# Kernel tuning notes

Hardware: AMD Instinct MI355X
Metric: run time of the kernel (lower is better)

The kernel has to match this reference:

```python
import jax, jax.numpy as jnp
import numpy as np

N_NODES = 50000
N_EDGES = 200000
NODE_DIM = 160     # node feat dim (divisible by 5 per wrapper slicing)
EDGE_DIM = 64      # latent edge feat dim
RAW_EDGE_DIM = 8   # raw geometric edge attributes
HID = 256          # hidden dim of edge/node update MLPs
ENC_HID = 128      # hidden dim of EASP edge encoder
N_ITER = 3
ENC_IN = 2 * NODE_DIM + RAW_EDGE_DIM                 # 328
EDGE_IN = 2 * 2 * NODE_DIM + 2 * EDGE_DIM            # 768 (reattach -> factor 2)
MSG_IN = 2 * NODE_DIM + EDGE_DIM                     # 384 (reattach node + edge)


def _ln(x, g, b):
    mu = jnp.mean(x, axis=-1, keepdims=True)
    v = jnp.var(x, axis=-1, keepdims=True)
    return (x - mu) * jax.lax.rsqrt(v + 1e-5) * g + b


def setup_inputs() -> dict:
    key = jax.random.key(0)
    ks = jax.random.split(key, 24)

    def w(k, shape):
        return (jax.random.normal(k, shape, jnp.float32) / np.sqrt(shape[0])).astype(jnp.float32)

    return {
        'x': jax.random.normal(ks[0], (N_NODES, NODE_DIM), jnp.float32),
        'edge_attr': jax.random.normal(ks[1], (N_EDGES, RAW_EDGE_DIM), jnp.float32),
        # EASP edge encoder MLP
        'enc_W1': w(ks[2], (ENC_IN, ENC_HID)), 'enc_b1': jnp.zeros((ENC_HID,), jnp.float32),
        'enc_W2': w(ks[3], (ENC_HID, EDGE_DIM)), 'enc_b2': jnp.zeros((EDGE_DIM,), jnp.float32),
        # EdgeCNN edge update MLP
        'eW1': w(ks[4], (EDGE_IN, HID)), 'eb1': jnp.zeros((HID,), jnp.float32),
        'eW2': w(ks[5], (HID, EDGE_DIM)), 'eb2': jnp.zeros((EDGE_DIM,), jnp.float32),
        # AttentionNodeUpdateNet: per-edge message MLP + attention vector + node out
        'mW1': w(ks[6], (MSG_IN, HID)), 'mb1': jnp.zeros((HID,), jnp.float32),
        'att_v': w(ks[7], (HID,)),
        'nW1': w(ks[8], (HID, NODE_DIM)), 'nb1': jnp.zeros((NODE_DIM,), jnp.float32),
        # shared LayerNorms (ModuleList([layer]*n_iter) shares one layer)
        'ln_ng': jnp.ones((NODE_DIM,), jnp.float32), 'ln_nb': jnp.zeros((NODE_DIM,), jnp.float32),
        'ln_eg': jnp.ones((EDGE_DIM,), jnp.float32), 'ln_eb': jnp.zeros((EDGE_DIM,), jnp.float32),
        'edge_row': jax.random.randint(ks[9], (N_EDGES,), 0, N_NODES, jnp.int32),
        'edge_col': jax.random.randint(ks[10], (N_EDGES,), 0, N_NODES, jnp.int32),
    }


def reference(x, edge_attr, enc_W1, enc_b1, enc_W2, enc_b2, eW1, eb1, eW2, eb2,
              mW1, mb1, att_v, nW1, nb1, ln_ng, ln_nb, ln_eg, ln_eb,
              edge_row, edge_col):
    row, col = edge_row, edge_col
    # edge encoder: gather endpoints, encode raw edge attrs
    init_edge = jnp.concatenate([x[row], x[col], edge_attr], axis=1)  # [E, 328]
    init_edge = jnp.maximum(init_edge @ enc_W1 + enc_b1, 0.0) @ enc_W2 + enc_b2  # [E, 64]

    node_lat, edge_lat = x, init_edge
    for _ in range(N_ITER):
        nl = jnp.concatenate([x, node_lat], axis=1)            # reattach initial node feats [N, 320]
        el = jnp.concatenate([init_edge, edge_lat], axis=1)    # reattach initial edge feats [E, 128]
        # edge update: gather-concat-MLP
        e_in = jnp.concatenate([nl[row], nl[col], el], axis=1)  # [E, 768]
        new_edge = jnp.maximum(e_in @ eW1 + eb1, 0.0) @ eW2 + eb2  # [E, 64]
        # node update: per-edge message + segment-softmax attention + scatter agg
        msg = jnp.maximum(jnp.concatenate([nl[col], new_edge], axis=1) @ mW1 + mb1, 0.0)  # [E, 256]
        logit = jax.nn.leaky_relu(msg @ att_v, 0.2)             # [E]
        smax = jax.ops.segment_max(logit, row, num_segments=N_NODES)
        ex = jnp.exp(logit - smax[row])
        den = jax.ops.segment_sum(ex, row, num_segments=N_NODES)
        alpha = ex / (den[row] + 1e-16)
        agg = jax.ops.segment_sum(alpha[:, None] * msg, row, num_segments=N_NODES)  # [N, 256]
        new_node = agg @ nW1 + nb1                              # [N, 160]
        # residual skip + (shared) LayerNorm
        node_lat = _ln(x + new_node, ln_ng, ln_nb)
        edge_lat = _ln(init_edge + new_edge, ln_eg, ln_eb)
    return node_lat, edge_lat
```

## Files before the change

### kernel.cpp

```cpp
#include <hip/hip_runtime.h>
#include <stdint.h>

#define N_NODES 50000
#define N_EDGES 200000
#define SCAN_B 512

typedef __bf16 bf16_t;
typedef bf16_t bf16x8 __attribute__((ext_vector_type(8)));
typedef float f32x4 __attribute__((ext_vector_type(4)));

__device__ __forceinline__ float bf2f(ushort h) {
  union { unsigned int u; float f; } c; c.u = ((unsigned int)h) << 16; return c.f;
}
__device__ __forceinline__ ushort f2bf(float f) {
  union { float f; unsigned int u; } c; c.f = f;
  unsigned int r = (c.u >> 16) & 1u;
  c.u += 0x7fffu + r;
  return (ushort)(c.u >> 16);
}
__device__ __forceinline__ float wave_sum(float v) {
#pragma unroll
  for (int m = 32; m > 0; m >>= 1) v += __shfl_xor(v, m, 64);
  return v;
}

__global__ void detect_k(const ushort* x, unsigned int* flag) {
  int i = blockIdx.x * 256 + threadIdx.x;
  unsigned int cnt = 0;
  for (int j = i; j < 1000000; j += 64 * 256) {
    ushort v = x[j];
    if (((v & 0x7F80u) == 0x7F80u) && (v & 0x7Fu)) cnt++;
  }
  if (cnt) atomicAdd(flag, cnt);
}

__global__ void cvt_in_k(const void* src, ushort* dst, int n, const unsigned int* flag) {
  int i = blockIdx.x * 256 + threadIdx.x;
  if (i >= n) return;
  if (*flag >= 2) dst[i] = f2bf(((const float*)src)[i]);
  else            dst[i] = ((const ushort*)src)[i];
}

__global__ void cvt_eattr_k(const void* src, const int* perm, ushort* dst,
                            const unsigned int* flag) {
  int i = blockIdx.x * 256 + threadIdx.x;
  if (i >= N_EDGES * 8) return;
  int e = i >> 3, j = i & 7;
  size_t o = (size_t)perm[e] * 8 + j;
  if (*flag >= 2) dst[i] = f2bf(((const float*)src)[o]);
  else            dst[i] = ((const ushort*)src)[o];
}

__global__ void transpose2_k(const void* W, ushort* Bt, int k0, int Ksrc, int Kpad,
                             int Wstride, const unsigned int* flag) {
  int k = blockIdx.x * 256 + threadIdx.x;
  int n = blockIdx.y;
  if (k >= Kpad) return;
  ushort v = 0;
  if (k < Ksrc) {
    if (*flag >= 2) v = f2bf(((const float*)W)[(size_t)(k0 + k) * Wstride + n]);
    else            v = ((const ushort*)W)[(size_t)(k0 + k) * Wstride + n];
  }
  Bt[(size_t)n * Kpad + k] = v;
}

__global__ void hist_k(const int* row, int* deg) {
  int e = blockIdx.x * 256 + threadIdx.x;
  if (e < N_EDGES) atomicAdd(&deg[row[e]], 1);
}
__global__ void scan_blk_k(const int* deg, int* off, int* bsum, int n) {
  __shared__ int s[SCAN_B];
  int i = blockIdx.x * SCAN_B + threadIdx.x;
  int v = (i < n) ? deg[i] : 0;
  s[threadIdx.x] = v;
  __syncthreads();
  for (int o = 1; o < SCAN_B; o <<= 1) {
    int t = (threadIdx.x >= o) ? s[threadIdx.x - o] : 0;
    __syncthreads();
    s[threadIdx.x] += t;
    __syncthreads();
  }
  if (i < n) off[i] = s[threadIdx.x] - v;
  if (threadIdx.x == SCAN_B - 1) bsum[blockIdx.x] = s[SCAN_B - 1];
}
__global__ void scan_top_k(int* bsum, int nb) {
  __shared__ int s[128];
  int v = (threadIdx.x < nb) ? bsum[threadIdx.x] : 0;
  s[threadIdx.x] = v;
  __syncthreads();
  for (int o = 1; o < 128; o <<= 1) {
    int t = (threadIdx.x >= o) ? s[threadIdx.x - o] : 0;
    __syncthreads();
    s[threadIdx.x] += t;
    __syncthreads();
  }
  if (threadIdx.x < nb) bsum[threadIdx.x] = s[threadIdx.x] - v;
}
__global__ void scan_add_k(int* off, const int* bsum, int n) {
  int i = blockIdx.x * 256 + threadIdx.x;
  if (i < n) off[i] += bsum[i >> 9];
  if (i == 0) off[n] = N_EDGES;
}
__global__ void fill_k(const int* row, const int* off, int* cur, int* perm) {
  int e = blockIdx.x * 256 + threadIdx.x;
  if (e >= N_EDGES) return;
  int r = row[e];
  int p = off[r] + atomicAdd(&cur[r], 1);
  perm[p] = e;
}
__global__ void gather_rc_k(const int* row, const int* col, const int* perm,
                            int* rs, int* cs) {
  int e = blockIdx.x * 256 + threadIdx.x;
  if (e >= N_EDGES) return;
  int o = perm[e];
  rs[e] = row[o];
  cs[e] = col[o];
}

struct GemmP {
  const ushort* X;
  const ushort* L;
  const ushort* E2;
  const float*  Af;
  const int* row;
  const int* col;
  const ushort* Bt;
  const ushort* bias;
  const ushort* Cr;
  const ushort* Cc;
  long cst;
  ushort* outb;  long ob_stride;
  ushort* outb2; long ob2_stride;
  ushort* outS;  long oS_stride;
  int nsplit;
  float*  outf;  long of_stride;
  long e2s;
  int M, K, Nw;
};

template <int MODE>
__device__ __forceinline__ uint4 load_a8(const GemmP& p, int e, int kg) {
  if (MODE == 0) {
    return *(const uint4*)(p.E2 + (size_t)e * p.e2s + kg);
  } else if (MODE == 5) {
    if (kg < 160) return *(const uint4*)(p.X + (size_t)e * 160 + kg);
    return *(const uint4*)(p.L + (size_t)e * 160 + (kg - 160));
  } else if (MODE == 7) {
    if (kg < 160) return *(const uint4*)(p.X + (size_t)e * 160 + kg);
    uint4 z; z.x = z.y = z.z = z.w = 0u; return z;
  } else if (MODE == 8) {
    if (kg < 8) return *(const uint4*)(p.E2 + (size_t)e * 8);
    uint4 z; z.x = z.y = z.z = z.w = 0u; return z;
  } else {
    const float* s = p.Af + (size_t)e * p.K + kg;
    f32x4 f0 = *(const f32x4*)s;
    f32x4 f1 = *(const f32x4*)(s + 4);
    union { ushort r[8]; uint4 u; } o;
    o.r[0] = f2bf(f0[0]); o.r[1] = f2bf(f0[1]); o.r[2] = f2bf(f0[2]); o.r[3] = f2bf(f0[3]);
    o.r[4] = f2bf(f1[0]); o.r[5] = f2bf(f1[1]); o.r[6] = f2bf(f1[2]); o.r[7] = f2bf(f1[3]);
    return o.u;
  }
}

template <int MODE, int CI, bool RELU, int NT, bool LNN>
__global__ __launch_bounds__(256) void gemm_k(GemmP p) {
  constexpr int BR = NT / 2;
  constexpr int NTC = NT * 16;
  constexpr int CIP = NTC + 8;
  __shared__ __align__(16) ushort smem[9216 + 1152 * NT];
  ushort* Asm = smem;
  ushort* Bsm = smem + 9216;
  const int t = threadIdx.x;
  const int w = t >> 6;
  const int l = t & 63;
  const int m0 = blockIdx.y * 128;
  const int n0 = blockIdx.x * NTC;

  const int srow = t >> 1;
  const int sph = (t & 1) << 5;
  int e = m0 + srow;
  if (e >= p.M) e = p.M - 1;

  int bn_[BR], bk_[BR];
#pragma unroll
  for (int j = 0; j < BR; j++) {
    int cid = j * 256 + t;
    bn_[j] = cid >> 3;
    bk_[j] = (cid & 7) << 3;
  }

  const int mq = l & 15;
  const int qd = l >> 4;

  uint4 ar[4];
  uint4 br[BR];
  auto load_tile = [&](int k0) {
#pragma unroll
    for (int j = 0; j < 4; j++)
      ar[j] = load_a8<MODE>(p, e, k0 + sph + j * 8);
#pragma unroll
    for (int j = 0; j < BR; j++)
      br[j] = *(const uint4*)(p.Bt + (size_t)(n0 + bn_[j]) * p.K + k0 + bk_[j]);
  };

  load_tile(0);

  f32x4 acc[2][NT] = {};
  if (CI) {
#pragma unroll
    for (int mt = 0; mt < 2; mt++) {
#pragma unroll
      for (int i = 0; i < 4; i++) {
        int r = m0 + w * 32 + mt * 16 + qd * 4 + i;
        if (r >= p.M) r = p.M - 1;
        const ushort* pc = p.Cc + (size_t)p.col[r] * p.cst + n0 + mq;
        const ushort* pr = nullptr;
        if (CI == 1) pr = p.Cr + (size_t)p.row[r] * p.cst + n0 + mq;
#pragma unroll
        for (int nt = 0; nt < NT; nt++) {
          float v = bf2f(pc[nt * 16]);
          if (CI == 1) v += bf2f(pr[nt * 16]);
          acc[mt][nt][i] = v;
        }
      }
    }
  }

  const int kiters = p.K >> 6;
  for (int kt = 0; kt < kiters; kt++) {
    __syncthreads();
#pragma unroll
    for (int j = 0; j < 4; j++)
      *(uint4*)&Asm[srow * 72 + sph + j * 8] = ar[j];
#pragma unroll
    for (int j = 0; j < BR; j++)
      *(uint4*)&Bsm[bn_[j] * 72 + bk_[j]] = br[j];
    if (kt + 1 < kiters) load_tile((kt + 1) << 6);
    __syncthreads();
#pragma unroll
    for (int ph = 0; ph < 2; ph++) {
      uint4 ra0 = *(const uint4*)&Asm[(w * 32 + mq) * 72 + ph * 32 + qd * 8];
      uint4 ra1 = *(const uint4*)&Asm[(w * 32 + 16 + mq) * 72 + ph * 32 + qd * 8];
      bf16x8 af0 = __builtin_bit_cast(bf16x8, ra0);
      bf16x8 af1 = __builtin_bit_cast(bf16x8, ra1);
#pragma unroll
      for (int nt = 0; nt < NT; nt++) {
        uint4 rb = *(const uint4*)&Bsm[(nt * 16 + mq) * 72 + ph * 32 + qd * 8];
        bf16x8 bfv = __builtin_bit_cast(bf16x8, rb);
        acc[0][nt] = __builtin_amdgcn_mfma_f32_16x16x32_bf16(af0, bfv, acc[0][nt], 0, 0, 0);
        acc[1][nt] = __builtin_amdgcn_mfma_f32_16x16x32_bf16(af1, bfv, acc[1][nt], 0, 0, 0);
      }
    }
  }

  if (MODE == 4) {
    if (LNN) {
#pragma unroll
      for (int mt = 0; mt < 2; mt++) {
#pragma unroll
        for (int i = 0; i < 4; i++) {
          int r = m0 + w * 32 + mt * 16 + qd * 4 + i;
          int rc = (r < p.M) ? r : p.M - 1;
          float vals[NT];
          float s = 0.0f;
#pragma unroll
          for (int nt = 0; nt < NT; nt++) {
            int c = n0 + nt * 16 + mq;
            float v = acc[mt][nt][i] + bf2f(p.bias[c]) +
                      bf2f(p.X[(size_t)rc * p.of_stride + c]);
            vals[nt] = v; s += v;
          }
#pragma unroll
          for (int m = 1; m <= 8; m <<= 1) s += __shfl_xor(s, m, 64);
          float mu = s * (1.0f / 160.0f);
          float ss = 0.0f;
#pragma unroll
          for (int nt = 0; nt < NT; nt++) { float d = vals[nt] - mu; ss += d * d; }
#pragma unroll
          for (int m = 1; m <= 8; m <<= 1) ss += __shfl_xor(ss, m, 64);
          float inv = rsqrtf(ss * (1.0f / 160.0f) + 1e-5f);
          if (r < p.M) {
#pragma unroll
            for (int nt = 0; nt < NT; nt++) {
              int c = n0 + nt * 16 + mq;
              float o = (vals[nt] - mu) * inv * bf2f(p.Cr[c]) + bf2f(p.Cc[c]);
              p.outb[(size_t)r * p.ob_stride + c] = f2bf(o);
            }
          }
        }
      }
    } else {
#pragma unroll
      for (int mt = 0; mt < 2; mt++) {
#pragma unroll
        for (int nt = 0; nt < NT; nt++) {
          int c = n0 + nt * 16 + mq;
          float bv = bf2f(p.bias[c]);
#pragma unroll
          for (int i = 0; i < 4; i++) {
            int r = m0 + w * 32 + mt * 16 + qd * 4 + i;
            if (r >= p.M) continue;
            float v = acc[mt][nt][i] + bv;
            if (RELU) v = fmaxf(v, 0.0f);
            p.outf[(size_t)r * p.of_stride + c] = v;
          }
        }
      }
    }
  } else {
    ushort* dst = p.outb;
    long dstr = p.ob_stride;
    int nb0 = n0;
    if (p.outS && n0 >= p.nsplit) { dst = p.outS; dstr = p.oS_stride; nb0 = n0 - p.nsplit; }
    __syncthreads();
    ushort* S = smem + w * (32 * CIP);
#pragma unroll
    for (int mt = 0; mt < 2; mt++) {
#pragma unroll
      for (int nt = 0; nt < NT; nt++) {
        float bv = bf2f(p.bias[n0 + nt * 16 + mq]);
#pragma unroll
        for (int i = 0; i < 4; i++) {
          float v = acc[mt][nt][i] + bv;
          if (RELU) v = fmaxf(v, 0.0f);
          S[(mt * 16 + qd * 4 + i) * CIP + nt * 16 + mq] = f2bf(v);
        }
      }
    }
    __syncthreads();
#pragma unroll
    for (int j = 0; j < NT; j++) {
      int flat = (j * 64 + l) * 8;
      int lr = flat / NTC, cc = flat % NTC;
      int r = m0 + w * 32 + lr;
      if (r < p.M) {
        uint4 v = *(const uint4*)&S[lr * CIP + cc];
        *(uint4*)(dst + (size_t)r * dstr + nb0 + cc) = v;
        if (p.outb2) *(uint4*)(p.outb2 + (size_t)r * p.ob2_stride + n0 + cc) = v;
      }
    }
  }
}

__global__ void copy_u4_k(const uint4* s, uint4* d, int n) {
  int i = blockIdx.x * 256 + threadIdx.x;
  if (i < n) d[i] = s[i];
}

__global__ void agg_csr_k(const ushort* msg, const ushort* att, const int* off,
                          float* agg) {
  int n = blockIdx.x * 4 + (threadIdx.x >> 6);
  int l = threadIdx.x & 63;
  if (n >= N_NODES) return;
  const int s0 = off[n], s1 = off[n + 1];
  ushort4 av = *(const ushort4*)(att + l * 4);
  const float a0 = bf2f(av.x), a1 = bf2f(av.y), a2 = bf2f(av.z), a3 = bf2f(av.w);
  float maxl = -1e30f;
  for (int j = s0; j < s1; j++) {
    ushort4 m = *(const ushort4*)(msg + (size_t)j * 256 + l * 4);
    float d = bf2f(m.x) * a0 + bf2f(m.y) * a1 + bf2f(m.z) * a2 + bf2f(m.w) * a3;
    d = wave_sum(d);
    float lg = (d > 0.0f) ? d : 0.2f * d;
    maxl = fmaxf(maxl, lg);
  }
  float den = 0.0f;
  f32x4 acc = {0.0f, 0.0f, 0.0f, 0.0f};
  for (int j = s0; j < s1; j++) {
    ushort4 m = *(const ushort4*)(msg + (size_t)j * 256 + l * 4);
    float m0 = bf2f(m.x), m1 = bf2f(m.y), m2 = bf2f(m.z), m3 = bf2f(m.w);
    float d = m0 * a0 + m1 * a1 + m2 * a2 + m3 * a3;
    d = wave_sum(d);
    float lg = (d > 0.0f) ? d : 0.2f * d;
    float ex = __expf(lg - maxl);
    den += ex;
    acc[0] += ex * m0; acc[1] += ex * m1; acc[2] += ex * m2; acc[3] += ex * m3;
  }
  float inv = 1.0f / (den + 1e-16f);
  f32x4 o = {acc[0] * inv, acc[1] * inv, acc[2] * inv, acc[3] * inv};
  *(f32x4*)(agg + (size_t)n * 256 + l * 4) = o;
}

__global__ void ln_edge_k(const ushort* g, const ushort* b, ushort* el) {
  int e = blockIdx.x * 4 + (threadIdx.x >> 6);
  int l = threadIdx.x & 63;
  if (e >= N_EDGES) return;
  float v = bf2f(el[(size_t)e * 128 + l]) + bf2f(el[(size_t)e * 128 + 64 + l]);
  float mu = wave_sum(v) * (1.0f / 64.0f);
  float d = v - mu;
  float var = wave_sum(d * d) * (1.0f / 64.0f);
  float inv = rsqrtf(var + 1e-5f);
  el[(size_t)e * 128 + 64 + l] = f2bf(d * inv * bf2f(g[l]) + bf2f(b[l]));
}

__global__ void out_node_k(const ushort* nlat, void* out, const unsigned int* flag) {
  int i = blockIdx.x * 256 + threadIdx.x;
  if (i >= N_NODES * 160) return;
  if (*flag >= 2) ((float*)out)[i] = bf2f(nlat[i]);
  else            ((ushort*)out)[i] = nlat[i];
}
__global__ void out_edge_k(const ushort* el, const int* perm, void* out,
                           const unsigned int* flag) {
  int i = blockIdx.x * 256 + threadIdx.x;
  if (i >= N_EDGES * 64) return;
  int e = i >> 6, c = i & 63;
  ushort v = el[(size_t)e * 128 + 64 + c];
  size_t o = (size_t)N_NODES * 160 + (size_t)perm[e] * 64 + c;
  if (*flag >= 2) ((float*)out)[o] = bf2f(v);
  else            ((ushort*)out)[o] = v;
}

extern "C" void kernel_launch(void* const* d_in, const int* in_sizes, int n_in,
                              void* d_out, int out_size, void* d_ws, size_t ws_size,
                              hipStream_t stream) {
  const void* x_r     = d_in[0];
  const void* eattr_r = d_in[1];
  const void* encW1   = d_in[2];
  const void* encb1_r = d_in[3];
  const void* encW2   = d_in[4];
  const void* encb2_r = d_in[5];
  const void* eW1     = d_in[6];
  const void* eb1_r   = d_in[7];
  const void* eW2     = d_in[8];
  const void* eb2_r   = d_in[9];
  const void* mW1     = d_in[10];
  const void* mb1_r   = d_in[11];
  const void* attv_r  = d_in[12];
  const void* nW1     = d_in[13];
  const void* nb1_r   = d_in[14];
  const void* lnng_r  = d_in[15];
  const void* lnnb_r  = d_in[16];
  const void* lneg_r  = d_in[17];
  const void* lneb_r  = d_in[18];
  const int* erow = (const int*)d_in[19];
  const int* ecol = (const int*)d_in[20];
  (void)in_sizes; (void)n_in;

  char* ws = (char*)d_ws;
  size_t off = 0;
  auto alloc = [&](size_t bytes) -> void* {
    void* p = ws + off;
    off = (off + bytes + 511) & ~(size_t)511;
    return p;
  };
  ushort* hm   = (ushort*)alloc((size_t)N_EDGES * 256 * 2);
  ushort* el   = (ushort*)alloc((size_t)N_EDGES * 128 * 2);
  float*  agg  = (float*)alloc((size_t)N_NODES * 256 * 4);
  ushort* xc   = (ushort*)alloc((size_t)N_NODES * 160 * 2);
  ushort* nlat = (ushort*)alloc((size_t)N_NODES * 160 * 2);
  ushort* Qc   = (ushort*)alloc((size_t)N_NODES * 256 * 2);
  int* degcur  = (int*)alloc((size_t)2 * N_NODES * 4);
  int* offcsr  = (int*)alloc((size_t)(N_NODES + 1) * 4);
  int* perm    = (int*)alloc((size_t)N_EDGES * 4);
  int* rs      = (int*)alloc((size_t)N_EDGES * 4);
  int* cs      = (int*)alloc((size_t)N_EDGES * 4);
  int* bsum    = (int*)alloc((size_t)128 * 4);
  ushort* BtPe = (ushort*)alloc((size_t)256 * 192 * 2);
  ushort* BtWenc = (ushort*)alloc((size_t)128 * 64 * 2);
  ushort* BtE2 = (ushort*)alloc((size_t)64 * 128 * 2);
  ushort* BtPQ = (ushort*)alloc((size_t)768 * 320 * 2);
  ushort* BtWe = (ushort*)alloc((size_t)256 * 128 * 2);
  ushort* Bte2 = (ushort*)alloc((size_t)64 * 256 * 2);
  ushort* BtWm = (ushort*)alloc((size_t)256 * 64 * 2);
  ushort* Btn1 = (ushort*)alloc((size_t)160 * 256 * 2);
  ushort* pool = (ushort*)alloc((size_t)4096 * 2);
  unsigned int* flag = (unsigned int*)alloc(64);
  ushort* msg = hm;
  ushort* eac  = (ushort*)agg;
  ushort* Penc = (ushort*)((char*)agg + (size_t)N_EDGES * 8 * 2);
  ushort* Prc  = (ushort*)agg;
  ushort* zb   = pool + 2048;

  ushort* encb1c = pool;        ushort* encb2c = pool + 128;
  ushort* eb1c   = pool + 192;  ushort* eb2c   = pool + 448;
  ushort* mb1c   = pool + 512;  ushort* attvc  = pool + 768;
  ushort* nb1c   = pool + 1024; ushort* lnngc  = pool + 1184;
  ushort* lnnbc  = pool + 1344; ushort* lnegc  = pool + 1504;
  ushort* lnebc  = pool + 1568;

  if (off > ws_size) {
    hipMemsetAsync(d_out, 0, (size_t)out_size * 2, stream);
    return;
  }

  hipMemsetAsync(flag, 0, 64, stream);
  hipMemsetAsync(pool, 0, 4096 * 2, stream);
  hipMemsetAsync(degcur, 0, (size_t)2 * N_NODES * 4, stream);

  detect_k<<<64, 256, 0, stream>>>((const ushort*)x_r, flag);

  {
    int* deg = degcur;
    int* cur = degcur + N_NODES;
    const int nb = (N_NODES + SCAN_B - 1) / SCAN_B;
    hist_k<<<(N_EDGES + 255) / 256, 256, 0, stream>>>(erow, deg);
    scan_blk_k<<<nb, SCAN_B, 0, stream>>>(deg, offcsr, bsum, N_NODES);
    scan_top_k<<<1, 128, 0, stream>>>(bsum, nb);
    scan_add_k<<<(N_NODES + 255) / 256, 256, 0, stream>>>(offcsr, bsum, N_NODES);
    fill_k<<<(N_EDGES + 255) / 256, 256, 0, stream>>>(erow, offcsr, cur, perm);
    gather_rc_k<<<(N_EDGES + 255) / 256, 256, 0, stream>>>(erow, ecol, perm, rs, cs);
  }

  cvt_in_k<<<(N_NODES * 160 + 255) / 256, 256, 0, stream>>>(x_r, xc, N_NODES * 160, flag);
  cvt_eattr_k<<<(N_EDGES * 8 + 255) / 256, 256, 0, stream>>>(eattr_r, perm, eac, flag);
  cvt_in_k<<<1, 256, 0, stream>>>(encb1_r, encb1c, 128, flag);
  cvt_in_k<<<1, 256, 0, stream>>>(encb2_r, encb2c, 64, flag);
  cvt_in_k<<<1, 256, 0, stream>>>(eb1_r, eb1c, 256, flag);
  cvt_in_k<<<1, 256, 0, stream>>>(eb2_r, eb2c, 64, flag);
  cvt_in_k<<<1, 256, 0, stream>>>(mb1_r, mb1c, 256, flag);
  cvt_in_k<<<1, 256, 0, stream>>>(attv_r, attvc, 256, flag);
  cvt_in_k<<<1, 256, 0, stream>>>(nb1_r, nb1c, 160, flag);
  cvt_in_k<<<1, 256, 0, stream>>>(lnng_r, lnngc, 160, flag);
  cvt_in_k<<<1, 256, 0, stream>>>(lnnb_r, lnnbc, 160, flag);
  cvt_in_k<<<1, 256, 0, stream>>>(lneg_r, lnegc, 64, flag);
  cvt_in_k<<<1, 256, 0, stream>>>(lneb_r, lnebc, 64, flag);

  transpose2_k<<<dim3(1, 128), 256, 0, stream>>>(encW1, BtPe,             0, 160, 192, 128, flag);
  transpose2_k<<<dim3(1, 128), 256, 0, stream>>>(encW1, BtPe + 128 * 192, 160, 160, 192, 128, flag);
  transpose2_k<<<dim3(1, 128), 256, 0, stream>>>(encW1, BtWenc,           320, 8, 64, 128, flag);
  transpose2_k<<<dim3(1, 64), 256, 0, stream>>>(encW2, BtE2, 0, 128, 128, 64, flag);
  transpose2_k<<<dim3(2, 256), 256, 0, stream>>>(eW1, BtPQ,             0, 320, 320, 256, flag);
  transpose2_k<<<dim3(2, 256), 256, 0, stream>>>(eW1, BtPQ + 256 * 320, 320, 320, 320, 256, flag);
  transpose2_k<<<dim3(2, 256), 256, 0, stream>>>(mW1, BtPQ + 512 * 320, 0, 320, 320, 256, flag);
  transpose2_k<<<dim3(1, 256), 256, 0, stream>>>(eW1, BtWe, 640, 128, 128, 256, flag);
  transpose2_k<<<dim3(1, 64), 256, 0, stream>>>(eW2, Bte2, 0, 256, 256, 64, flag);
  transpose2_k<<<dim3(1, 256), 256, 0, stream>>>(mW1, BtWm, 320, 64, 64, 256, flag);
  transpose2_k<<<dim3(1, 160), 256, 0, stream>>>(nW1, Btn1, 0, 256, 256, 160, flag);

  copy_u4_k<<<(N_NODES * 160 / 8 + 255) / 256, 256, 0, stream>>>(
      (const uint4*)xc, (uint4*)nlat, N_NODES * 160 / 8);

  const int gE = (N_EDGES + 127) / 128;
  const int gN = (N_NODES + 127) / 128;

  {
    GemmP p{};
    p.X = xc; p.Bt = BtPe; p.bias = zb;
    p.outb = Penc; p.ob_stride = 256;
    p.M = N_NODES; p.K = 192; p.Nw = 256;
    gemm_k<7, 0, false, 8, false><<<dim3(2, gN), 256, 0, stream>>>(p);
  }
  {
    GemmP p{};
    p.E2 = eac; p.row = rs; p.col = cs;
    p.Cr = Penc; p.Cc = Penc + 128; p.cst = 256;
    p.Bt = BtWenc; p.bias = encb1c;
    p.outb = hm; p.ob_stride = 128;
    p.M = N_EDGES; p.K = 64; p.Nw = 128;
    gemm_k<8, 1, true, 8, false><<<dim3(1, gE), 256, 0, stream>>>(p);
  }
  {
    GemmP p{};
    p.E2 = hm; p.e2s = 128; p.Bt = BtE2; p.bias = encb2c;
    p.outb = el; p.ob_stride = 128;
    p.outb2 = el + 64; p.ob2_stride = 128;
    p.M = N_EDGES; p.K = 128; p.Nw = 64;
    gemm_k<0, 0, false, 4, false><<<dim3(1, gE), 256, 0, stream>>>(p);
  }

  for (int it = 0; it < 3; it++) {
    {
      GemmP p{};
      p.X = xc; p.L = nlat; p.Bt = BtPQ; p.bias = zb;
      p.outb = Prc; p.ob_stride = 512;
      p.outS = Qc; p.oS_stride = 256; p.nsplit = 512;
      p.M = N_NODES; p.K = 320; p.Nw = 768;
      gemm_k<5, 0, false, 8, false><<<dim3(6, gN), 256, 0, stream>>>(p);
    }
    {
      GemmP p{};
      p.E2 = el; p.e2s = 128; p.row = rs; p.col = cs;
      p.Cr = Prc; p.Cc = Prc + 256; p.cst = 512;
      p.Bt = BtWe; p.bias = eb1c;
      p.outb = hm; p.ob_stride = 256;
      p.M = N_EDGES; p.K = 128; p.Nw = 256;
      gemm_k<0, 1, true, 8, false><<<dim3(2, gE), 256, 0, stream>>>(p);
    }
    {
      GemmP p{};
      p.E2 = hm; p.e2s = 256; p.Bt = Bte2; p.bias = eb2c;
      p.outb = el + 64; p.ob_stride = 128;
      p.M = N_EDGES; p.K = 256; p.Nw = 64;
      gemm_k<0, 0, false, 4, false><<<dim3(1, gE), 256, 0, stream>>>(p);
    }
    {
      GemmP p{};
      p.E2 = el + 64; p.e2s = 128; p.row = rs; p.col = cs;
      p.Cc = Qc; p.cst = 256;
      p.Bt = BtWm; p.bias = mb1c;
      p.outb = msg; p.ob_stride = 256;
      p.M = N_EDGES; p.K = 64; p.Nw = 256;
      gemm_k<0, 2, true, 8, false><<<dim3(2, gE), 256, 0, stream>>>(p);
    }
    ln_edge_k<<<N_EDGES / 4, 256, 0, stream>>>(lnegc, lnebc, el);
    agg_csr_k<<<(N_NODES + 3) / 4, 256, 0, stream>>>(msg, attvc, offcsr, agg);
    {
      GemmP p{};
      p.Af = agg; p.Bt = Btn1; p.bias = nb1c;
      p.X = xc; p.of_stride = 160;
      p.Cr = lnngc; p.Cc = lnnbc;
      p.outb = nlat; p.ob_stride = 160;
      p.M = N_NODES; p.K = 256; p.Nw = 160;
      gemm_k<4, 0, false, 10, true><<<dim3(1, gN), 256, 0, stream>>>(p);
    }
  }

  out_node_k<<<(N_NODES * 160 + 255) / 256, 256, 0, stream>>>(nlat, d_out, flag);
  out_edge_k<<<(N_EDGES * 64 + 255) / 256, 256, 0, stream>>>(el, perm, d_out, flag);
  (void)out_size;
}
```

Before: 1.764 ms.

## Fuse two-layer edge update MLP into one kernel and swizzle GEMM block order

Adds edge12_k, which computes the edge-update hidden layer (gathered node projections plus edge-latent GEMM, ReLU) and keeps the 256-wide hidden tile in shared memory with an XOR swizzle, then runs the second GEMM from there. This removes the [E,256] hidden tensor round trip through global memory and one launch per iteration. It also adds an optional 1D grid swizzle to gemm_k so that the N-blocks sharing an M panel run close together, improving L2 reuse of A rows. The fused kernel reads the second-layer weights straight from global memory and uses 512 threads with 64KB of shared memory, which may lower occupancy.

```diff
diff --git a/kernel.cpp b/kernel.cpp
--- a/kernel.cpp
+++ b/kernel.cpp
@@ -136,6 +136,7 @@
   float*  outf;  long of_stride;
   long e2s;
   int M, K, Nw;
+  int swzn;
 };
 
 template <int MODE>
@@ -173,8 +174,18 @@
   const int t = threadIdx.x;
   const int w = t >> 6;
   const int l = t & 63;
-  const int m0 = blockIdx.y * 128;
-  const int n0 = blockIdx.x * NTC;
+  int m0, n0;
+  if (p.swzn) {
+    int b = blockIdx.x;
+    int panel = (b & 7) + ((b >> 3) / p.swzn) * 8;
+    int nb = (b >> 3) % p.swzn;
+    if (panel * 128 >= p.M) return;
+    m0 = panel * 128;
+    n0 = nb * NTC;
+  } else {
+    m0 = blockIdx.y * 128;
+    n0 = blockIdx.x * NTC;
+  }
 
   const int srow = t >> 1;
   const int sph = (t & 1) << 5;
@@ -339,6 +350,128 @@
         if (p.outb2) *(uint4*)(p.outb2 + (size_t)r * p.ob2_stride + n0 + cc) = v;
       }
     }
+  }
+}
+
+__global__ __launch_bounds__(512) void edge12_k(
+    const ushort* el, const int* rs, const int* cs, const ushort* Prc,
+    const ushort* BtWe, const ushort* eb1, const ushort* Bte2, const ushort* eb2,
+    ushort* elw, int M) {
+  __shared__ __align__(16) ushort smem[32768];
+  ushort* Asm = smem;
+  ushort* Bsm = smem + 9216;
+  const int t = threadIdx.x;
+  const int w = t >> 6;
+  const int l = t & 63;
+  const int m0 = blockIdx.x * 128;
+  const int mq = l & 15;
+  const int qd = l >> 4;
+
+  const int arow = t >> 2;
+  const int aph = (t & 3) << 4;
+  int ea = m0 + arow;
+  if (ea >= M) ea = M - 1;
+  int bn_[4], bk_[4];
+#pragma unroll
+  for (int j = 0; j < 4; j++) {
+    int cid = j * 512 + t;
+    bn_[j] = cid >> 3;
+    bk_[j] = (cid & 7) << 3;
+  }
+
+  uint4 ar[2], br[4];
+  auto load_tile = [&](int k0) {
+#pragma unroll
+    for (int j = 0; j < 2; j++)
+      ar[j] = *(const uint4*)(el + (size_t)ea * 128 + k0 + aph + j * 8);
+#pragma unroll
+    for (int j = 0; j < 4; j++)
+      br[j] = *(const uint4*)(BtWe + (size_t)bn_[j] * 128 + k0 + bk_[j]);
+  };
+  load_tile(0);
+
+  f32x4 acc[16] = {};
+#pragma unroll
+  for (int i = 0; i < 4; i++) {
+    int r = m0 + w * 16 + qd * 4 + i;
+    if (r >= M) r = M - 1;
+    const ushort* pc = Prc + (size_t)cs[r] * 512 + 256 + mq;
+    const ushort* pr = Prc + (size_t)rs[r] * 512 + mq;
+#pragma unroll
+    for (int nt = 0; nt < 16; nt++)
+      acc[nt][i] = bf2f(pc[nt * 16]) + bf2f(pr[nt * 16]);
+  }
+
+#pragma unroll
+  for (int kt = 0; kt < 2; kt++) {
+    __syncthreads();
+#pragma unroll
+    for (int j = 0; j < 2; j++)
+      *(uint4*)&Asm[arow * 72 + aph + j * 8] = ar[j];
+#pragma unroll
+    for (int j = 0; j < 4; j++)
+      *(uint4*)&Bsm[bn_[j] * 72 + bk_[j]] = br[j];
+    if (kt == 0) load_tile(64);
+    __syncthreads();
+#pragma unroll
+    for (int ph = 0; ph < 2; ph++) {
+      uint4 ra = *(const uint4*)&Asm[(w * 16 + mq) * 72 + ph * 32 + qd * 8];
+      bf16x8 af = __builtin_bit_cast(bf16x8, ra);
+#pragma unroll
+      for (int nt = 0; nt < 16; nt++) {
+        uint4 rb = *(const uint4*)&Bsm[(nt * 16 + mq) * 72 + ph * 32 + qd * 8];
+        bf16x8 bfv = __builtin_bit_cast(bf16x8, rb);
+        acc[nt] = __builtin_amdgcn_mfma_f32_16x16x32_bf16(af, bfv, acc[nt], 0, 0, 0);
+      }
+    }
+  }
+
+  __syncthreads();
+  ushort* S = smem + w * 4096;
+#pragma unroll
+  for (int nt = 0; nt < 16; nt++) {
+    float bv = bf2f(eb1[nt * 16 + mq]);
+#pragma unroll
+    for (int i = 0; i < 4; i++) {
+      int row = qd * 4 + i;
+      float v = fmaxf(acc[nt][i] + bv, 0.0f);
+      int bcol = ((nt * 16 + mq) * 2) ^ ((row & 7) << 4);
+      S[row * 256 + (bcol >> 1)] = f2bf(v);
+    }
+  }
+  __syncthreads();
+
+  f32x4 acc2[4] = {};
+#pragma unroll
+  for (int ks = 0; ks < 8; ks++) {
+    int bco = ((ks * 32 + qd * 8) * 2) ^ ((mq & 7) << 4);
+    uint4 ra2 = *(const uint4*)&S[mq * 256 + (bco >> 1)];
+    bf16x8 af2 = __builtin_bit_cast(bf16x8, ra2);
+#pragma unroll
+    for (int nt2 = 0; nt2 < 4; nt2++) {
+      uint4 rb2 = *(const uint4*)(Bte2 + (size_t)(nt2 * 16 + mq) * 256 + ks * 32 + qd * 8);
+      bf16x8 bf2v = __builtin_bit_cast(bf16x8, rb2);
+      acc2[nt2] = __builtin_amdgcn_mfma_f32_16x16x32_bf16(af2, bf2v, acc2[nt2], 0, 0, 0);
+    }
+  }
+  __syncthreads();
+
+  ushort* S2 = smem + w * 1152;
+#pragma unroll
+  for (int nt2 = 0; nt2 < 4; nt2++) {
+    float bv2 = bf2f(eb2[nt2 * 16 + mq]);
+#pragma unroll
+    for (int i = 0; i < 4; i++)
+      S2[(qd * 4 + i) * 72 + nt2 * 16 + mq] = f2bf(acc2[nt2][i] + bv2);
+  }
+  __syncthreads();
+#pragma unroll
+  for (int j = 0; j < 2; j++) {
+    int flat = (j * 64 + l) * 8;
+    int lr = flat >> 6, cc = flat & 63;
+    int r = m0 + w * 16 + lr;
+    if (r < M)
+      *(uint4*)(elw + (size_t)r * 128 + 64 + cc) = *(const uint4*)&S2[lr * 72 + cc];
   }
 }
 
@@ -531,13 +664,15 @@
 
   const int gE = (N_EDGES + 127) / 128;
   const int gN = (N_NODES + 127) / 128;
+  const int gN8 = 8 * ((gN + 7) / 8);
+  const int gE8 = 8 * ((gE + 7) / 8);
 
   {
     GemmP p{};
     p.X = xc; p.Bt = BtPe; p.bias = zb;
     p.outb = Penc; p.ob_stride = 256;
-    p.M = N_NODES; p.K = 192; p.Nw = 256;
-    gemm_k<7, 0, false, 8, false><<<dim3(2, gN), 256, 0, stream>>>(p);
+    p.M = N_NODES; p.K = 192; p.Nw = 256; p.swzn = 2;
+    gemm_k<7, 0, false, 8, false><<<gN8 * 2, 256, 0, stream>>>(p);
   }
   {
     GemmP p{};
@@ -563,33 +698,19 @@
       p.X = xc; p.L = nlat; p.Bt = BtPQ; p.bias = zb;
       p.outb = Prc; p.ob_stride = 512;
       p.outS = Qc; p.oS_stride = 256; p.nsplit = 512;
-      p.M = N_NODES; p.K = 320; p.Nw = 768;
-      gemm_k<5, 0, false, 8, false><<<dim3(6, gN), 256, 0, stream>>>(p);
-    }
-    {
-      GemmP p{};
-      p.E2 = el; p.e2s = 128; p.row = rs; p.col = cs;
-      p.Cr = Prc; p.Cc = Prc + 256; p.cst = 512;
-      p.Bt = BtWe; p.bias = eb1c;
-      p.outb = hm; p.ob_stride = 256;
-      p.M = N_EDGES; p.K = 128; p.Nw = 256;
-      gemm_k<0, 1, true, 8, false><<<dim3(2, gE), 256, 0, stream>>>(p);
-    }
-    {
-      GemmP p{};
-      p.E2 = hm; p.e2s = 256; p.Bt = Bte2; p.bias = eb2c;
-      p.outb = el + 64; p.ob_stride = 128;
-      p.M = N_EDGES; p.K = 256; p.Nw = 64;
-      gemm_k<0, 0, false, 4, false><<<dim3(1, gE), 256, 0, stream>>>(p);
-    }
+      p.M = N_NODES; p.K = 320; p.Nw = 768; p.swzn = 6;
+      gemm_k<5, 0, false, 8, false><<<gN8 * 6, 256, 0, stream>>>(p);
+    }
+    edge12_k<<<gE, 512, 0, stream>>>(el, rs, cs, Prc, BtWe, eb1c, Bte2, eb2c,
+                                     el, N_EDGES);
     {
       GemmP p{};
       p.E2 = el + 64; p.e2s = 128; p.row = rs; p.col = cs;
       p.Cc = Qc; p.cst = 256;
       p.Bt = BtWm; p.bias = mb1c;
       p.outb = msg; p.ob_stride = 256;
-      p.M = N_EDGES; p.K = 64; p.Nw = 256;
-      gemm_k<0, 2, true, 8, false><<<dim3(2, gE), 256, 0, stream>>>(p);
+      p.M = N_EDGES; p.K = 64; p.Nw = 256; p.swzn = 2;
+      gemm_k<0, 2, true, 8, false><<<gE8 * 2, 256, 0, stream>>>(p);
     }
     ln_edge_k<<<N_EDGES / 4, 256, 0, stream>>>(lnegc, lnebc, el);
     agg_csr_k<<<(N_NODES + 3) / 4, 256, 0, stream>>>(msg, attvc, offcsr, agg);
```

New measurement: 1.979 ms. 12.2% more time.
